# Performance work log

Measured on AMD Instinct MI355X. Metric: run time of the kernel, lower is better.

The kernel has to match this reference:

```python
import jax, jax.numpy as jnp
import numpy as np
from jax import lax

DIM = 96
SHIFT_SIZE = 3
EPS = 1e-5


def conv1x1(x, w, b):
    # x: [B,C,H,W], w: [O,C], b: [O]
    return jnp.einsum('bchw,oc->bohw', x, w) + b[None, :, None, None]


def groupnorm1(x, w, b):
    # GroupNorm(1, C): normalize over (C,H,W) per sample; affine per channel.
    mu = jnp.mean(x, axis=(1, 2, 3), keepdims=True)
    var = jnp.mean(jnp.square(x - mu), axis=(1, 2, 3), keepdims=True)
    xn = (x - mu) * lax.rsqrt(var + EPS)
    return xn * w[None, :, None, None] + b[None, :, None, None]


def axial_shift(x, axis):
    # Faithful to Shift: zero-pad spatial dims by pad, chunk channels into
    # SHIFT_SIZE groups, roll chunk i by shift in range(-pad, pad+1) along
    # `axis`, then crop back to HxW. Because |shift| <= pad, roll+crop equals
    # a static slice of the zero-padded tensor (no wraparound touches output).
    B, C, H, W = x.shape
    pad = SHIFT_SIZE // 2
    xp = jnp.pad(x, ((0, 0), (0, 0), (pad, pad), (pad, pad)))
    chunks = jnp.split(xp, SHIFT_SIZE, axis=1)
    cs = C // SHIFT_SIZE
    outs = []
    for xc, s in zip(chunks, range(-pad, pad + 1)):
        start = [0, 0, pad, pad]
        start[axis] = pad - s
        outs.append(lax.dynamic_slice(xc, start, (B, cs, H, W)))
    return jnp.concatenate(outs, axis=1)


def setup_inputs() -> dict:
    key = jax.random.key(0)
    ks = jax.random.split(key, 11)
    B, C, H, W = 32, DIM, 112, 112
    sc = 1.0 / np.sqrt(C)
    inp = {
        'x': jax.random.normal(ks[0], (B, C, H, W), dtype=jnp.float32),
        'w1': jax.random.normal(ks[1], (C, C), dtype=jnp.float32) * sc,
        'b1': jnp.zeros((C,), jnp.float32),
        'w21': jax.random.normal(ks[2], (C, C), dtype=jnp.float32) * sc,
        'b21': jnp.zeros((C,), jnp.float32),
        'w22': jax.random.normal(ks[3], (C, C), dtype=jnp.float32) * sc,
        'b22': jnp.zeros((C,), jnp.float32),
        'w3': jax.random.normal(ks[4], (C, C), dtype=jnp.float32) * sc,
        'b3': jnp.zeros((C,), jnp.float32),
        'gn1_w': jnp.ones((C,), jnp.float32),
        'gn1_b': jnp.zeros((C,), jnp.float32),
        'gn2_w': jnp.ones((C,), jnp.float32),
        'gn2_b': jnp.zeros((C,), jnp.float32),
    }
    return inp


def reference(x, w1, b1, w21, b21, w22, b22, w3, b3, gn1_w, gn1_b, gn2_w, gn2_b):
    gelu = lambda t: jax.nn.gelu(t, approximate=False)
    h = conv1x1(x, w1, b1)
    h = groupnorm1(h, gn1_w, gn1_b)
    h = gelu(h)
    h_lr = axial_shift(h, axis=3)  # shift along W
    h_td = axial_shift(h, axis=2)  # shift along H
    h = gelu(conv1x1(h_lr, w21, b21)) + gelu(conv1x1(h_td, w22, b22))
    h = groupnorm1(h, gn2_w, gn2_b)
    return conv1x1(h, w3, b3)
```

## Files before the change

### kernel.cpp

```cpp
#include <hip/hip_runtime.h>
#include <math.h>

#define CCH 96
#define HH 112
#define WW 112
#define HWSZ 12544
#define NB 32
#define PIX 64
#define NBLK 196
#define EPSV 1e-5f
#define APITCH 120
#define TPITCH 72
#define TPITCHF 68
#define ROWC 96

typedef __attribute__((ext_vector_type(8))) short bf16x8;
typedef __attribute__((ext_vector_type(4))) float f32x4;
typedef __attribute__((ext_vector_type(8))) unsigned short u16x8;

__device__ __forceinline__ unsigned short f2bf(float f) {
    union { float f; unsigned u; } v; v.f = f;
    unsigned r = v.u + 0x7fffu + ((v.u >> 16) & 1u);
    return (unsigned short)(r >> 16);
}
__device__ __forceinline__ float bf2f(unsigned short h) {
    union { unsigned u; float f; } v; v.u = ((unsigned)h) << 16;
    return v.f;
}
__device__ __forceinline__ unsigned cvt_pk_bf16(float lo, float hi) {
    unsigned r;
    asm("v_cvt_pk_bf16_f32 %0, %1, %2" : "=v"(r) : "v"(lo), "v"(hi));
    return r;
}
__device__ __forceinline__ float gelu_f(float x) {
    const float K = 2.3022082f;
    float u = x * x;
    float p = x * fmaf(0.044715f, u, 1.0f);
    float e = __builtin_amdgcn_exp2f(p * K);
    float r = __builtin_amdgcn_rcpf(e + 1.0f);
    return x - x * r;
}

__device__ __forceinline__ void block_reduce_write(float sum, float sumsq,
                                                   float* part, int slot) {
    #pragma unroll
    for (int off = 32; off > 0; off >>= 1) {
        sum += __shfl_down(sum, off);
        sumsq += __shfl_down(sumsq, off);
    }
    __shared__ float ls[8];
    const int wid = threadIdx.x >> 6, lane = threadIdx.x & 63;
    if (lane == 0) { ls[wid] = sum; ls[4 + wid] = sumsq; }
    __syncthreads();
    if (threadIdx.x == 0) {
        part[slot * 2 + 0] = ls[0] + ls[1] + ls[2] + ls[3];
        part[slot * 2 + 1] = ls[4] + ls[5] + ls[6] + ls[7];
    }
}

__device__ __forceinline__ void stats_reduce(const float* __restrict__ part,
                                             int b, float* sh_mu, float* sh_inv) {
    const int t = threadIdx.x;
    if (t < 64) {
        float s = 0.f, q = 0.f;
        for (int i = t; i < NBLK; i += 64) {
            s += part[(b * NBLK + i) * 2 + 0];
            q += part[(b * NBLK + i) * 2 + 1];
        }
        #pragma unroll
        for (int off = 32; off > 0; off >>= 1) {
            s += __shfl_down(s, off);
            q += __shfl_down(q, off);
        }
        if (t == 0) {
            const float n = (float)CCH * (float)HWSZ;
            const float mu = s / n;
            const float var = q / n - mu * mu;
            *sh_mu = mu;
            *sh_inv = rsqrtf(var + EPSV);
        }
    }
}

__global__ void k_prep(const float* __restrict__ w1, const float* __restrict__ w21,
                       const float* __restrict__ w22,
                       unsigned short* __restrict__ Bp) {
    const int t = blockIdx.x * 256 + threadIdx.x;
    if (t >= 3 * 18 * 512) return;
    const int j  = t & 7;
    const int l  = (t >> 3) & 63;
    const int s  = t >> 9;
    const int k0 = s % 3;
    const int n0 = (s / 3) % 6;
    const int m  = s / 18;
    const float* w = (m == 0) ? w1 : (m == 1) ? w21 : w22;
    const int n = n0 * 16 + (l & 15);
    const int k = k0 * 32 + (l >> 4) * 8 + j;
    Bp[t] = f2bf(w[n * CCH + k]);
}

__global__ __launch_bounds__(256) void k_conv1(
        const float* __restrict__ x, const unsigned short* __restrict__ Bp,
        const float* __restrict__ b1, unsigned short* __restrict__ h1t,
        float* __restrict__ part) {
    __shared__ unsigned short smem[64 * APITCH];
    unsigned short* Asd = smem;
    unsigned short* Tsd = smem;

    const int b = blockIdx.y;
    const int hw0 = blockIdx.x * PIX;
    const int wid = __builtin_amdgcn_readfirstlane(threadIdx.x >> 6);
    const int lane = threadIdx.x & 63;

    const float* xb = x + (size_t)b * CCH * HWSZ + hw0;
    #pragma unroll
    for (int i = 0; i < 24; i += 2) {
        const int c = wid * 24 + i;
        *(unsigned*)&Asd[lane * APITCH + c] =
            cvt_pk_bf16(xb[(size_t)c * HWSZ + lane], xb[(size_t)(c + 1) * HWSZ + lane]);
    }
    __syncthreads();

    bf16x8 a[3];
    const int arow = (wid * 16 + (lane & 15)) * APITCH;
    const int acol = (lane >> 4) * 8;
    #pragma unroll
    for (int k0 = 0; k0 < 3; ++k0)
        a[k0] = *(const bf16x8*)&Asd[arow + k0 * 32 + acol];
    __syncthreads();

    f32x4 acc[6];
    #pragma unroll
    for (int n0 = 0; n0 < 6; ++n0) {
        const float bias = b1[n0 * 16 + (lane & 15)];
        acc[n0] = (f32x4){bias, bias, bias, bias};
        #pragma unroll
        for (int k0 = 0; k0 < 3; ++k0) {
            const bf16x8 bf = *(const bf16x8*)(Bp + (n0 * 3 + k0) * 512 + lane * 8);
            acc[n0] = __builtin_amdgcn_mfma_f32_16x16x32_bf16(a[k0], bf, acc[n0], 0, 0, 0);
        }
    }

    float sum = 0.f, sumsq = 0.f;
    const int p0 = wid * 16 + (lane >> 4) * 4;
    #pragma unroll
    for (int n0 = 0; n0 < 6; ++n0) {
        const int o = n0 * 16 + (lane & 15);
        #pragma unroll
        for (int r = 0; r < 4; ++r) {
            const float v = acc[n0][r];
            sum += v; sumsq += v * v;
        }
        const unsigned lo = cvt_pk_bf16(acc[n0][0], acc[n0][1]);
        const unsigned hi = cvt_pk_bf16(acc[n0][2], acc[n0][3]);
        *(uint2*)&Tsd[o * TPITCH + p0] = make_uint2(lo, hi);
    }
    __syncthreads();

    unsigned short* ob = h1t + ((size_t)b * HWSZ + hw0) * ROWC;
    #pragma unroll
    for (int it = 0; it < 3; ++it) {
        const int u = threadIdx.x + it * 256;
        const int pr = u / 12;
        const int c16 = (u % 12) * 8;
        unsigned r0 = (unsigned)Tsd[(c16 + 0) * TPITCH + pr] |
                      ((unsigned)Tsd[(c16 + 1) * TPITCH + pr] << 16);
        unsigned r1 = (unsigned)Tsd[(c16 + 2) * TPITCH + pr] |
                      ((unsigned)Tsd[(c16 + 3) * TPITCH + pr] << 16);
        unsigned r2 = (unsigned)Tsd[(c16 + 4) * TPITCH + pr] |
                      ((unsigned)Tsd[(c16 + 5) * TPITCH + pr] << 16);
        unsigned r3 = (unsigned)Tsd[(c16 + 6) * TPITCH + pr] |
                      ((unsigned)Tsd[(c16 + 7) * TPITCH + pr] << 16);
        *(uint4*)&ob[(size_t)pr * ROWC + c16] = make_uint4(r0, r1, r2, r3);
    }
    block_reduce_write(sum, sumsq, part, b * NBLK + blockIdx.x);
}

__global__ __launch_bounds__(256) void k_gact(
        unsigned short* __restrict__ g, const float* __restrict__ part,
        const float* __restrict__ gw, const float* __restrict__ gb) {
    const int b = blockIdx.y;
    __shared__ __align__(16) float ts[CCH];
    __shared__ __align__(16) float th[CCH];
    __shared__ float sh_mu, sh_inv;
    stats_reduce(part, b, &sh_mu, &sh_inv);
    __syncthreads();
    const int t = threadIdx.x;
    if (t < CCH) {
        const float sc = sh_inv * gw[t];
        ts[t] = sc;
        th[t] = gb[t] - sh_mu * sc;
    }
    __syncthreads();
    unsigned short* gb_ = g + (size_t)b * HWSZ * ROWC;
    #pragma unroll
    for (int i = 0; i < 4; ++i) {
        const int v = blockIdx.x * 1024 + i * 256 + t;
        const int c0 = (v % 12) * 8;
        const u16x8 gv = *(const u16x8*)&gb_[(size_t)v * 8];
        const f32x4 s0 = *(const f32x4*)&ts[c0];
        const f32x4 s1 = *(const f32x4*)&ts[c0 + 4];
        const f32x4 h0 = *(const f32x4*)&th[c0];
        const f32x4 h1 = *(const f32x4*)&th[c0 + 4];
        float f[8];
        #pragma unroll
        for (int j = 0; j < 4; ++j) {
            f[j]     = gelu_f(fmaf(bf2f(gv[j]),     s0[j], h0[j]));
            f[j + 4] = gelu_f(fmaf(bf2f(gv[j + 4]), s1[j], h1[j]));
        }
        const unsigned r0 = cvt_pk_bf16(f[0], f[1]);
        const unsigned r1 = cvt_pk_bf16(f[2], f[3]);
        const unsigned r2 = cvt_pk_bf16(f[4], f[5]);
        const unsigned r3 = cvt_pk_bf16(f[6], f[7]);
        *(uint4*)&gb_[(size_t)v * 8] = make_uint4(r0, r1, r2, r3);
    }
}

__global__ __launch_bounds__(256) void k_mid(
        const unsigned short* __restrict__ gt,
        const unsigned short* __restrict__ BpA, const unsigned short* __restrict__ BpB,
        const float* __restrict__ b21, const float* __restrict__ b22,
        unsigned short* __restrict__ h2t, float* __restrict__ part) {
    __shared__ unsigned short Tsd[CCH * TPITCH];

    const int b = blockIdx.y;
    const int hw0 = blockIdx.x * PIX;
    const int wid = __builtin_amdgcn_readfirstlane(threadIdx.x >> 6);
    const int lane = threadIdx.x & 63;
    const int prow = hw0 + wid * 16 + (lane & 15);
    const int w = prow % WW;
    const int hrow = prow / WW;
    const int acol8 = (lane >> 4) * 8;
    const unsigned short* gb_ = gt + (size_t)b * HWSZ * ROWC;

    bf16x8 alr[3], atd[3];
    const bf16x8 zf = (bf16x8){0, 0, 0, 0, 0, 0, 0, 0};
    #pragma unroll
    for (int k0 = 0; k0 < 3; ++k0) {
        const int d = (k0 == 0) ? 1 : (k0 == 1) ? 0 : -1;
        if (d == 0) {
            bf16x8 f0 = *(const bf16x8*)(gb_ + (size_t)prow * ROWC + k0 * 32 + acol8);
            alr[k0] = f0;
            atd[k0] = f0;
        } else {
            const bool okL = (unsigned)(w + d) < WW;
            const bool okT = (unsigned)(hrow + d) < HH;
            const int pL = okL ? prow + d : prow;
            const int pT = okT ? prow + d * WW : prow;
            bf16x8 fl = *(const bf16x8*)(gb_ + (size_t)pL * ROWC + k0 * 32 + acol8);
            bf16x8 ft = *(const bf16x8*)(gb_ + (size_t)pT * ROWC + k0 * 32 + acol8);
            alr[k0] = okL ? fl : zf;
            atd[k0] = okT ? ft : zf;
        }
    }

    f32x4 accA[6], accB[6];
    #pragma unroll
    for (int n0 = 0; n0 < 6; ++n0) {
        const float biasA = b21[n0 * 16 + (lane & 15)];
        const float biasB = b22[n0 * 16 + (lane & 15)];
        accA[n0] = (f32x4){biasA, biasA, biasA, biasA};
        accB[n0] = (f32x4){biasB, biasB, biasB, biasB};
        #pragma unroll
        for (int k0 = 0; k0 < 3; ++k0) {
            const bf16x8 bA = *(const bf16x8*)(BpA + (n0 * 3 + k0) * 512 + lane * 8);
            const bf16x8 bB = *(const bf16x8*)(BpB + (n0 * 3 + k0) * 512 + lane * 8);
            accA[n0] = __builtin_amdgcn_mfma_f32_16x16x32_bf16(alr[k0], bA, accA[n0], 0, 0, 0);
            accB[n0] = __builtin_amdgcn_mfma_f32_16x16x32_bf16(atd[k0], bB, accB[n0], 0, 0, 0);
        }
    }

    float sum = 0.f, sumsq = 0.f;
    const int p0 = wid * 16 + (lane >> 4) * 4;
    #pragma unroll
    for (int n0 = 0; n0 < 6; ++n0) {
        const int o = n0 * 16 + (lane & 15);
        float vv[4];
        #pragma unroll
        for (int r = 0; r < 4; ++r) {
            const float v = gelu_f(accA[n0][r]) + gelu_f(accB[n0][r]);
            sum += v; sumsq += v * v;
            vv[r] = v;
        }
        const unsigned lo = cvt_pk_bf16(vv[0], vv[1]);
        const unsigned hi = cvt_pk_bf16(vv[2], vv[3]);
        *(uint2*)&Tsd[o * TPITCH + p0] = make_uint2(lo, hi);
    }
    __syncthreads();

    unsigned short* ob = h2t + ((size_t)b * HWSZ + hw0) * ROWC;
    #pragma unroll
    for (int it = 0; it < 3; ++it) {
        const int u = threadIdx.x + it * 256;
        const int pr = u / 12;
        const int c16 = (u % 12) * 8;
        unsigned r0 = (unsigned)Tsd[(c16 + 0) * TPITCH + pr] |
                      ((unsigned)Tsd[(c16 + 1) * TPITCH + pr] << 16);
        unsigned r1 = (unsigned)Tsd[(c16 + 2) * TPITCH + pr] |
                      ((unsigned)Tsd[(c16 + 3) * TPITCH + pr] << 16);
        unsigned r2 = (unsigned)Tsd[(c16 + 4) * TPITCH + pr] |
                      ((unsigned)Tsd[(c16 + 5) * TPITCH + pr] << 16);
        unsigned r3 = (unsigned)Tsd[(c16 + 6) * TPITCH + pr] |
                      ((unsigned)Tsd[(c16 + 7) * TPITCH + pr] << 16);
        *(uint4*)&ob[(size_t)pr * ROWC + c16] = make_uint4(r0, r1, r2, r3);
    }
    block_reduce_write(sum, sumsq, part, b * NBLK + blockIdx.x);
}

__global__ void k_wprep(const float* __restrict__ w3, const float* __restrict__ b3,
                        const float* __restrict__ part,
                        const float* __restrict__ gw, const float* __restrict__ gb,
                        unsigned short* __restrict__ W3p, float* __restrict__ biasp) {
    const int b = blockIdx.x;
    __shared__ float ts[CCH], th[CCH];
    __shared__ float sh_mu, sh_inv;
    stats_reduce(part, b, &sh_mu, &sh_inv);
    __syncthreads();
    const int t = threadIdx.x;
    if (t < CCH) {
        const float sc = sh_inv * gw[t];
        ts[t] = sc;
        th[t] = gb[t] - sh_mu * sc;
    }
    __syncthreads();
    unsigned short* Wb = W3p + b * 9216;
    #pragma unroll
    for (int i = 0; i < 36; ++i) {
        const int idx = t + i * 256;
        const int j = idx & 7;
        const int l = (idx >> 3) & 63;
        const int s = idx >> 9;
        const int k0 = s % 3, n0 = s / 3;
        const int n = n0 * 16 + (l & 15);
        const int k = k0 * 32 + (l >> 4) * 8 + j;
        Wb[idx] = f2bf(w3[n * CCH + k] * ts[k]);
    }
    if (t < CCH) {
        float a = b3[t];
        for (int c = 0; c < CCH; ++c) a = fmaf(w3[t * CCH + c], th[c], a);
        biasp[b * CCH + t] = a;
    }
}

__global__ __launch_bounds__(256) void k_out(
        const unsigned short* __restrict__ h2t, const unsigned short* __restrict__ W3p,
        const float* __restrict__ biasp, float* __restrict__ out) {
    __shared__ float Tf[CCH * TPITCHF];

    const int b = blockIdx.y;
    const int hw0 = blockIdx.x * PIX;
    const int wid = __builtin_amdgcn_readfirstlane(threadIdx.x >> 6);
    const int lane = threadIdx.x & 63;
    const int prow = hw0 + wid * 16 + (lane & 15);
    const int acol8 = (lane >> 4) * 8;

    const unsigned short* hb = h2t + (size_t)b * HWSZ * ROWC;
    bf16x8 a[3];
    #pragma unroll
    for (int k0 = 0; k0 < 3; ++k0)
        a[k0] = *(const bf16x8*)(hb + (size_t)prow * ROWC + k0 * 32 + acol8);

    const unsigned short* Bb = W3p + b * 9216;
    f32x4 acc[6];
    #pragma unroll
    for (int n0 = 0; n0 < 6; ++n0) {
        const float bias = biasp[b * CCH + n0 * 16 + (lane & 15)];
        acc[n0] = (f32x4){bias, bias, bias, bias};
        #pragma unroll
        for (int k0 = 0; k0 < 3; ++k0) {
            const bf16x8 bf = *(const bf16x8*)(Bb + (n0 * 3 + k0) * 512 + lane * 8);
            acc[n0] = __builtin_amdgcn_mfma_f32_16x16x32_bf16(a[k0], bf, acc[n0], 0, 0, 0);
        }
    }

    const int p0 = wid * 16 + (lane >> 4) * 4;
    #pragma unroll
    for (int n0 = 0; n0 < 6; ++n0) {
        const int o = n0 * 16 + (lane & 15);
        *(f32x4*)&Tf[o * TPITCHF + p0] = acc[n0];
    }
    __syncthreads();

    float* op = out + (size_t)b * CCH * HWSZ + hw0;
    #pragma unroll
    for (int it = 0; it < 6; ++it) {
        const int o = it * 16 + (threadIdx.x >> 4);
        const int p = (threadIdx.x & 15) * 4;
        *(f32x4*)&op[(size_t)o * HWSZ + p] = *(const f32x4*)&Tf[o * TPITCHF + p];
    }
}

extern "C" void kernel_launch(void* const* d_in, const int* in_sizes, int n_in,
                              void* d_out, int out_size, void* d_ws, size_t ws_size,
                              hipStream_t stream) {
    const float* x    = (const float*)d_in[0];
    const float* w1   = (const float*)d_in[1];
    const float* b1   = (const float*)d_in[2];
    const float* w21  = (const float*)d_in[3];
    const float* b21  = (const float*)d_in[4];
    const float* w22  = (const float*)d_in[5];
    const float* b22  = (const float*)d_in[6];
    const float* w3   = (const float*)d_in[7];
    const float* b3   = (const float*)d_in[8];
    const float* gn1w = (const float*)d_in[9];
    const float* gn1b = (const float*)d_in[10];
    const float* gn2w = (const float*)d_in[11];
    const float* gn2b = (const float*)d_in[12];

    char* base = (char*)d_ws;
    unsigned short* Bp    = (unsigned short*)base;
    float*          part  = (float*)(base + 73728);
    unsigned short* W3p   = (unsigned short*)(base + 131072);
    float*          biasp = (float*)(base + 720896);
    unsigned short* h2t   = (unsigned short*)(base + 1048576);
    unsigned short* h1t   = (unsigned short*)d_out;

    dim3 grid(NBLK, NB), blk(256);
    k_prep<<<dim3(108), blk, 0, stream>>>(w1, w21, w22, Bp);
    k_conv1<<<grid, blk, 0, stream>>>(x, Bp, b1, h1t, part);
    k_gact<<<dim3(147, NB), blk, 0, stream>>>(h1t, part, gn1w, gn1b);
    k_mid<<<grid, blk, 0, stream>>>(h1t, Bp + 18 * 512, Bp + 36 * 512,
                                    b21, b22, h2t, part);
    k_wprep<<<dim3(NB), blk, 0, stream>>>(w3, b3, part, gn2w, gn2b, W3p, biasp);
    k_out<<<grid, blk, 0, stream>>>(h2t, W3p, biasp, (float*)d_out);
}
```

Measured before the change: 202.2 us.

## Fuse GroupNorm1+GELU into mid kernel using 8x8 spatial tiles with halo

Removes the separate k_gact pass, which read and rewrote the whole bf16 h1 tensor. The mid kernel now tiles the image into 8x8 pixel patches and loads a 10x10 halo into LDS. It applies the GroupNorm scale/shift and GELU while loading, then reads shifted neighbours from LDS instead of issuing global gathers. Costs are recomputing GELU on halo pixels (100 vs 64), a larger LDS footprint, an extra barrier, and output writes that are no longer contiguous per block (8 rows of 8 pixels).

```diff
diff --git a/kernel.cpp b/kernel.cpp
--- a/kernel.cpp
+++ b/kernel.cpp
@@ -13,6 +13,7 @@
 #define TPITCH 72
 #define TPITCHF 68
 #define ROWC 96
+#define HPITCH 104
 
 typedef __attribute__((ext_vector_type(8))) short bf16x8;
 typedef __attribute__((ext_vector_type(4))) float f32x4;
@@ -176,83 +177,78 @@
     block_reduce_write(sum, sumsq, part, b * NBLK + blockIdx.x);
 }
 
-__global__ __launch_bounds__(256) void k_gact(
-        unsigned short* __restrict__ g, const float* __restrict__ part,
-        const float* __restrict__ gw, const float* __restrict__ gb) {
-    const int b = blockIdx.y;
+__global__ __launch_bounds__(256) void k_mid(
+        const unsigned short* __restrict__ h1t,
+        const unsigned short* __restrict__ BpA, const unsigned short* __restrict__ BpB,
+        const float* __restrict__ b21, const float* __restrict__ b22,
+        const float* __restrict__ part1,
+        const float* __restrict__ gw, const float* __restrict__ gb,
+        unsigned short* __restrict__ h2t, float* __restrict__ part2) {
+    __shared__ unsigned short Hs[100 * HPITCH];
+    unsigned short* Tsd = Hs;
     __shared__ __align__(16) float ts[CCH];
     __shared__ __align__(16) float th[CCH];
     __shared__ float sh_mu, sh_inv;
-    stats_reduce(part, b, &sh_mu, &sh_inv);
-    __syncthreads();
-    const int t = threadIdx.x;
-    if (t < CCH) {
-        const float sc = sh_inv * gw[t];
-        ts[t] = sc;
-        th[t] = gb[t] - sh_mu * sc;
-    }
-    __syncthreads();
-    unsigned short* gb_ = g + (size_t)b * HWSZ * ROWC;
-    #pragma unroll
-    for (int i = 0; i < 4; ++i) {
-        const int v = blockIdx.x * 1024 + i * 256 + t;
-        const int c0 = (v % 12) * 8;
-        const u16x8 gv = *(const u16x8*)&gb_[(size_t)v * 8];
-        const f32x4 s0 = *(const f32x4*)&ts[c0];
-        const f32x4 s1 = *(const f32x4*)&ts[c0 + 4];
-        const f32x4 h0 = *(const f32x4*)&th[c0];
-        const f32x4 h1 = *(const f32x4*)&th[c0 + 4];
-        float f[8];
-        #pragma unroll
-        for (int j = 0; j < 4; ++j) {
-            f[j]     = gelu_f(fmaf(bf2f(gv[j]),     s0[j], h0[j]));
-            f[j + 4] = gelu_f(fmaf(bf2f(gv[j + 4]), s1[j], h1[j]));
-        }
-        const unsigned r0 = cvt_pk_bf16(f[0], f[1]);
-        const unsigned r1 = cvt_pk_bf16(f[2], f[3]);
-        const unsigned r2 = cvt_pk_bf16(f[4], f[5]);
-        const unsigned r3 = cvt_pk_bf16(f[6], f[7]);
-        *(uint4*)&gb_[(size_t)v * 8] = make_uint4(r0, r1, r2, r3);
-    }
-}
-
-__global__ __launch_bounds__(256) void k_mid(
-        const unsigned short* __restrict__ gt,
-        const unsigned short* __restrict__ BpA, const unsigned short* __restrict__ BpB,
-        const float* __restrict__ b21, const float* __restrict__ b22,
-        unsigned short* __restrict__ h2t, float* __restrict__ part) {
-    __shared__ unsigned short Tsd[CCH * TPITCH];
 
     const int b = blockIdx.y;
-    const int hw0 = blockIdx.x * PIX;
-    const int wid = __builtin_amdgcn_readfirstlane(threadIdx.x >> 6);
-    const int lane = threadIdx.x & 63;
-    const int prow = hw0 + wid * 16 + (lane & 15);
-    const int w = prow % WW;
-    const int hrow = prow / WW;
+    const int oy = (blockIdx.x / 14) * 8;
+    const int ox = (blockIdx.x % 14) * 8;
+    const int tid = threadIdx.x;
+
+    stats_reduce(part1, b, &sh_mu, &sh_inv);
+    __syncthreads();
+    if (tid < CCH) {
+        const float sc = sh_inv * gw[tid];
+        ts[tid] = sc;
+        th[tid] = gb[tid] - sh_mu * sc;
+    }
+    __syncthreads();
+
+    const unsigned short* hb1 = h1t + (size_t)b * HWSZ * ROWC;
+    #pragma unroll
+    for (int it = 0; it < 5; ++it) {
+        const int idx = tid + it * 256;
+        if (idx < 1200) {
+            const int r = idx / 12;
+            const int c0 = (idx % 12) * 8;
+            const int hh = oy - 1 + r / 10;
+            const int ww = ox - 1 + r % 10;
+            unsigned r0 = 0, r1 = 0, r2 = 0, r3 = 0;
+            if ((unsigned)hh < HH && (unsigned)ww < WW) {
+                const u16x8 gv = *(const u16x8*)&hb1[((size_t)hh * WW + ww) * ROWC + c0];
+                const f32x4 s0 = *(const f32x4*)&ts[c0];
+                const f32x4 s1 = *(const f32x4*)&ts[c0 + 4];
+                const f32x4 t0 = *(const f32x4*)&th[c0];
+                const f32x4 t1 = *(const f32x4*)&th[c0 + 4];
+                float f[8];
+                #pragma unroll
+                for (int j = 0; j < 4; ++j) {
+                    f[j]     = gelu_f(fmaf(bf2f(gv[j]),     s0[j], t0[j]));
+                    f[j + 4] = gelu_f(fmaf(bf2f(gv[j + 4]), s1[j], t1[j]));
+                }
+                r0 = cvt_pk_bf16(f[0], f[1]);
+                r1 = cvt_pk_bf16(f[2], f[3]);
+                r2 = cvt_pk_bf16(f[4], f[5]);
+                r3 = cvt_pk_bf16(f[6], f[7]);
+            }
+            *(uint4*)&Hs[r * HPITCH + c0] = make_uint4(r0, r1, r2, r3);
+        }
+    }
+    __syncthreads();
+
+    const int wid = __builtin_amdgcn_readfirstlane(tid >> 6);
+    const int lane = tid & 63;
+    const int p = wid * 16 + (lane & 15);
+    const int hr = ((p >> 3) + 1) * 10 + (p & 7) + 1;
     const int acol8 = (lane >> 4) * 8;
-    const unsigned short* gb_ = gt + (size_t)b * HWSZ * ROWC;
 
     bf16x8 alr[3], atd[3];
-    const bf16x8 zf = (bf16x8){0, 0, 0, 0, 0, 0, 0, 0};
-    #pragma unroll
-    for (int k0 = 0; k0 < 3; ++k0) {
-        const int d = (k0 == 0) ? 1 : (k0 == 1) ? 0 : -1;
-        if (d == 0) {
-            bf16x8 f0 = *(const bf16x8*)(gb_ + (size_t)prow * ROWC + k0 * 32 + acol8);
-            alr[k0] = f0;
-            atd[k0] = f0;
-        } else {
-            const bool okL = (unsigned)(w + d) < WW;
-            const bool okT = (unsigned)(hrow + d) < HH;
-            const int pL = okL ? prow + d : prow;
-            const int pT = okT ? prow + d * WW : prow;
-            bf16x8 fl = *(const bf16x8*)(gb_ + (size_t)pL * ROWC + k0 * 32 + acol8);
-            bf16x8 ft = *(const bf16x8*)(gb_ + (size_t)pT * ROWC + k0 * 32 + acol8);
-            alr[k0] = okL ? fl : zf;
-            atd[k0] = okT ? ft : zf;
-        }
-    }
+    alr[0] = *(const bf16x8*)&Hs[(hr + 1)  * HPITCH +  0 + acol8];
+    alr[1] = *(const bf16x8*)&Hs[hr        * HPITCH + 32 + acol8];
+    alr[2] = *(const bf16x8*)&Hs[(hr - 1)  * HPITCH + 64 + acol8];
+    atd[0] = *(const bf16x8*)&Hs[(hr + 10) * HPITCH +  0 + acol8];
+    atd[1] = alr[1];
+    atd[2] = *(const bf16x8*)&Hs[(hr - 10) * HPITCH + 64 + acol8];
 
     f32x4 accA[6], accB[6];
     #pragma unroll
@@ -269,6 +265,7 @@
             accB[n0] = __builtin_amdgcn_mfma_f32_16x16x32_bf16(atd[k0], bB, accB[n0], 0, 0, 0);
         }
     }
+    __syncthreads();
 
     float sum = 0.f, sumsq = 0.f;
     const int p0 = wid * 16 + (lane >> 4) * 4;
@@ -288,12 +285,13 @@
     }
     __syncthreads();
 
-    unsigned short* ob = h2t + ((size_t)b * HWSZ + hw0) * ROWC;
+    unsigned short* ob = h2t + (size_t)b * HWSZ * ROWC;
     #pragma unroll
     for (int it = 0; it < 3; ++it) {
-        const int u = threadIdx.x + it * 256;
+        const int u = tid + it * 256;
         const int pr = u / 12;
         const int c16 = (u % 12) * 8;
+        const size_t gp = (size_t)(oy + (pr >> 3)) * WW + ox + (pr & 7);
         unsigned r0 = (unsigned)Tsd[(c16 + 0) * TPITCH + pr] |
                       ((unsigned)Tsd[(c16 + 1) * TPITCH + pr] << 16);
         unsigned r1 = (unsigned)Tsd[(c16 + 2) * TPITCH + pr] |
@@ -302,19 +300,19 @@
                       ((unsigned)Tsd[(c16 + 5) * TPITCH + pr] << 16);
         unsigned r3 = (unsigned)Tsd[(c16 + 6) * TPITCH + pr] |
                       ((unsigned)Tsd[(c16 + 7) * TPITCH + pr] << 16);
-        *(uint4*)&ob[(size_t)pr * ROWC + c16] = make_uint4(r0, r1, r2, r3);
-    }
-    block_reduce_write(sum, sumsq, part, b * NBLK + blockIdx.x);
+        *(uint4*)&ob[gp * ROWC + c16] = make_uint4(r0, r1, r2, r3);
+    }
+    block_reduce_write(sum, sumsq, part2, b * NBLK + blockIdx.x);
 }
 
 __global__ void k_wprep(const float* __restrict__ w3, const float* __restrict__ b3,
-                        const float* __restrict__ part,
+                        const float* __restrict__ part2,
                         const float* __restrict__ gw, const float* __restrict__ gb,
                         unsigned short* __restrict__ W3p, float* __restrict__ biasp) {
     const int b = blockIdx.x;
     __shared__ float ts[CCH], th[CCH];
     __shared__ float sh_mu, sh_inv;
-    stats_reduce(part, b, &sh_mu, &sh_inv);
+    stats_reduce(part2, b, &sh_mu, &sh_inv);
     __syncthreads();
     const int t = threadIdx.x;
     if (t < CCH) {
@@ -409,18 +407,18 @@
 
     char* base = (char*)d_ws;
     unsigned short* Bp    = (unsigned short*)base;
-    float*          part  = (float*)(base + 73728);
-    unsigned short* W3p   = (unsigned short*)(base + 131072);
-    float*          biasp = (float*)(base + 720896);
+    float*          part1 = (float*)(base + 73728);
+    float*          part2 = (float*)(base + 123904);
+    unsigned short* W3p   = (unsigned short*)(base + 180224);
+    float*          biasp = (float*)(base + 770048);
     unsigned short* h2t   = (unsigned short*)(base + 1048576);
     unsigned short* h1t   = (unsigned short*)d_out;
 
-    dim3 grid(NBLK, NB), blk(256);
+    dim3 blk(256);
     k_prep<<<dim3(108), blk, 0, stream>>>(w1, w21, w22, Bp);
-    k_conv1<<<grid, blk, 0, stream>>>(x, Bp, b1, h1t, part);
-    k_gact<<<dim3(147, NB), blk, 0, stream>>>(h1t, part, gn1w, gn1b);
-    k_mid<<<grid, blk, 0, stream>>>(h1t, Bp + 18 * 512, Bp + 36 * 512,
-                                    b21, b22, h2t, part);
-    k_wprep<<<dim3(NB), blk, 0, stream>>>(w3, b3, part, gn2w, gn2b, W3p, biasp);
-    k_out<<<grid, blk, 0, stream>>>(h2t, W3p, biasp, (float*)d_out);
-}
+    k_conv1<<<dim3(NBLK, NB), blk, 0, stream>>>(x, Bp, b1, h1t, part1);
+    k_mid<<<dim3(196, NB), blk, 0, stream>>>(h1t, Bp + 18 * 512, Bp + 36 * 512,
+                                             b21, b22, part1, gn1w, gn1b, h2t, part2);
+    k_wprep<<<dim3(NB), blk, 0, stream>>>(w3, b3, part2, gn2w, gn2b, W3p, biasp);
+    k_out<<<dim3(NBLK, NB), blk, 0, stream>>>(h2t, W3p, biasp, (float*)d_out);
+}
```

Result: faster. 186.4 us (-7.9%).
